# Performance work log

Measured on AMD Instinct MI355X. Metric: run time of the kernel, lower is better.

## Reference

```python
import jax, jax.numpy as jnp
import numpy as np

DIM = 768
NUM_HEADS = 16
D = DIM // NUM_HEADS  # 48


def setup_inputs() -> dict:
    key = jax.random.key(0)
    ks = jax.random.split(key, 7)
    x = jax.random.normal(ks[0], (4, 4096, DIM), dtype=jnp.float32)
    # Linear weights stored as [in, out] for x @ W + b
    s = 1.0 / np.sqrt(DIM)
    Wq = jax.random.uniform(ks[1], (DIM, D), jnp.float32, -s, s)
    Wk = jax.random.uniform(ks[2], (DIM, D), jnp.float32, -s, s)
    Wv = jax.random.uniform(ks[3], (DIM, D), jnp.float32, -s, s)
    bq = jax.random.uniform(ks[4], (D,), jnp.float32, -s, s)
    bk = jax.random.uniform(ks[5], (D,), jnp.float32, -s, s)
    bv = jax.random.uniform(ks[6], (D,), jnp.float32, -s, s)
    return {"x": x, "Wq": Wq, "bq": bq, "Wk": Wk, "bk": bk, "Wv": Wv, "bv": bv}


def reference(x, Wq, bq, Wk, bk, Wv, bv):
    # q, k, v: [B, S, D]
    q = x @ Wq + bq
    k = x @ Wk + bk
    v = x @ Wv + bv
    scale = 1.0 / jnp.sqrt(jnp.asarray(D, dtype=q.dtype))
    # scores: [B, S_q, S_k]
    scores = jnp.einsum("bqd,bkd->bqk", q, k) * scale
    # NOTE: softmax over dim=1 = the QUERY axis (faithful to original torch code)
    qk = jax.nn.softmax(scores, axis=1)
    # dropout is identity in eval mode (deterministic reference)
    attn = jnp.einsum("bqk,bkd->bqd", qk, v)
    return attn
```

## Files before the change

### kernel.cpp

```cpp
#include <hip/hip_runtime.h>
#include <hip/hip_bf16.h>

#define NB 4
#define SEQ 4096
#define CDIM 768
#define HD 48

typedef __attribute__((ext_vector_type(8))) __bf16 bf16x8;
typedef __attribute__((ext_vector_type(16))) float f32x16;

static constexpr float SCALE_LOG2E = 0.20823542135164923f;

__device__ __forceinline__ bf16x8 ldg8(const __hip_bfloat16* p) {
    uint4 u = *reinterpret_cast<const uint4*>(p);
    bf16x8 r;
    __builtin_memcpy(&r, &u, 16);
    return r;
}
__device__ __forceinline__ unsigned pk2(float lo, float hi) {
    const __hip_bfloat16 a = __float2bfloat16(lo);
    const __hip_bfloat16 b = __float2bfloat16(hi);
    unsigned short ua, ub;
    __builtin_memcpy(&ua, &a, 2);
    __builtin_memcpy(&ub, &b, 2);
    return (unsigned)ua | ((unsigned)ub << 16);
}
__device__ __forceinline__ bf16x8 mk8(unsigned w0, unsigned w1, unsigned w2, unsigned w3) {
    const uint4 u = make_uint4(w0, w1, w2, w3);
    bf16x8 r;
    __builtin_memcpy(&r, &u, 16);
    return r;
}
__device__ __forceinline__ void plswap(unsigned& a, unsigned& b) {
    asm volatile("v_permlane32_swap_b32 %0, %1" : "+v"(a), "+v"(b));
}
__device__ __forceinline__ size_t fragOff(int tile, int s, int h) {
    return (((size_t)tile * 3 + s) * 2 + h) * 256;
}

__global__ __launch_bounds__(256) void prep_kernel(
    const float* __restrict__ Wq, const float* __restrict__ Wk,
    const float* __restrict__ Wv,
    const float* __restrict__ bq, const float* __restrict__ bk,
    const float* __restrict__ bv,
    __hip_bfloat16* __restrict__ Wf, float* __restrict__ bias)
{
    const int g = blockIdx.x * 256 + threadIdx.x;
    if (g < 15360) {
        const int rem  = g % 3072;
        const int nt   = g / 3072;
        const int ks   = rem >> 6;
        const int l2   = rem & 63;
        const int hh   = l2 >> 5;
        const int lane = l2 & 31;
        const int n    = nt * 32 + lane;
        const float* src = (n < 48) ? Wq : (n < 96) ? Wk : (n < 144) ? Wv : nullptr;
        const int col = (n < 48) ? n : (n < 96) ? (n - 48) : (n - 96);
        #pragma unroll
        for (int j = 0; j < 8; ++j) {
            const int k = ks * 16 + hh * 8 + j;
            const float wv = src ? src[(size_t)k * HD + col] : 0.0f;
            Wf[(size_t)g * 8 + j] = __float2bfloat16(wv);
        }
    }
    if (blockIdx.x == 0 && threadIdx.x < 160) {
        const int t = threadIdx.x;
        bias[t] = (t < 48) ? bq[t] : (t < 96) ? bk[t - 48] : (t < 144) ? bv[t - 96] : 0.0f;
    }
}

__global__ __launch_bounds__(320) void proj_kernel(
    const float* __restrict__ x,
    const __hip_bfloat16* __restrict__ Wf, const float* __restrict__ bias,
    __hip_bfloat16* __restrict__ Qf, __hip_bfloat16* __restrict__ Kf,
    float* __restrict__ Vf)
{
    __shared__ __hip_bfloat16 xs[48 * 512];

    const int t   = threadIdx.x;
    const int w   = t >> 6;
    const int l   = t & 63;
    const int lo5 = l & 31, h = l >> 5;
    const int mt  = blockIdx.x;
    const int m0  = mt * 32;

    const float* xb = x + (size_t)m0 * CDIM;
    #pragma unroll
    for (int i = 0; i < 20; ++i) {
        const int c = i * 320 + t;
        if (c < 6144) {
            const int r   = c / 192;
            const int pos = c % 192;
            const int k   = pos * 4;
            const float4 v = *reinterpret_cast<const float4*>(xb + (size_t)r * CDIM + k);
            const int ks = k >> 4, hh = (k >> 3) & 1, j = k & 7;
            const uint2 d = make_uint2(pk2(v.x, v.y), pk2(v.z, v.w));
            *reinterpret_cast<uint2*>(&xs[ks * 512 + (hh * 32 + r) * 8 + j]) = d;
        }
    }
    __syncthreads();

    const __hip_bfloat16* bp = Wf + (size_t)w * 24576 + l * 8;
    f32x16 acc = {};
    #pragma unroll 8
    for (int ks = 0; ks < 48; ++ks) {
        bf16x8 a;
        __builtin_memcpy(&a, &xs[ks * 512 + l * 8], 16);
        const bf16x8 b = ldg8(bp + (size_t)ks * 512);
        __builtin_amdgcn_s_setprio(1);
        acc = __builtin_amdgcn_mfma_f32_32x32x16_bf16(a, b, acc, 0, 0, 0);
        __builtin_amdgcn_s_setprio(0);
    }

    const int n_g = w * 32 + lo5;
    const float bs = bias[n_g];
    if (n_g < 96) {
        const bool isQ = (n_g < 48);
        const int d  = isQ ? n_g : n_g - 48;
        const int s  = d >> 4;
        const int hf = (d >> 3) & 1;
        __hip_bfloat16* base = (isQ ? Qf : Kf) + fragOff(mt, s, hf) + (d & 7);
        #pragma unroll
        for (int r = 0; r < 16; ++r) {
            const int mrow = (r & 3) + 8 * (r >> 2) + 4 * h;
            float val = acc[r] + bs;
            if (isQ) val *= SCALE_LOG2E;
            base[mrow * 8] = __float2bfloat16(val);
        }
    } else if (n_g < 144) {
        const int d = n_g - 96;
        #pragma unroll
        for (int r = 0; r < 16; ++r) {
            const int m = m0 + (r & 3) + 8 * (r >> 2) + 4 * h;
            Vf[(size_t)m * HD + d] = acc[r] + bs;
        }
    }
}

__global__ __launch_bounds__(512) void stats_kernel(
    const __hip_bfloat16* __restrict__ Qf, const __hip_bfloat16* __restrict__ Kf,
    const float* __restrict__ Vf, __hip_bfloat16* __restrict__ Vt)
{
    __shared__ float part[8][32];
    __shared__ float linv[32];

    const int t   = threadIdx.x;
    const int w   = t >> 6;
    const int l   = t & 63;
    const int lo5 = l & 31, h = l >> 5;
    const int b       = blockIdx.y;
    const int ktile_l = blockIdx.x;
    const int ktile   = b * 128 + ktile_l;

    bf16x8 ka[3];
    #pragma unroll
    for (int s = 0; s < 3; ++s)
        ka[s] = ldg8(Kf + fragOff(ktile, s, h) + lo5 * 8);

    float lsum[16];
    #pragma unroll
    for (int r = 0; r < 16; ++r) lsum[r] = 0.0f;

    const int qt0 = b * 128 + w * 16;
    #pragma unroll 2
    for (int qq = 0; qq < 16; ++qq) {
        bf16x8 qb[3];
        #pragma unroll
        for (int s = 0; s < 3; ++s)
            qb[s] = ldg8(Qf + fragOff(qt0 + qq, s, h) + lo5 * 8);
        f32x16 acc = {};
        __builtin_amdgcn_s_setprio(1);
        #pragma unroll
        for (int s = 0; s < 3; ++s)
            acc = __builtin_amdgcn_mfma_f32_32x32x16_bf16(ka[s], qb[s], acc, 0, 0, 0);
        __builtin_amdgcn_s_setprio(0);
        #pragma unroll
        for (int r = 0; r < 16; ++r) lsum[r] += __builtin_amdgcn_exp2f(acc[r]);
    }

    #pragma unroll
    for (int r = 0; r < 16; ++r) {
        lsum[r] += __shfl_xor(lsum[r], 1);
        lsum[r] += __shfl_xor(lsum[r], 2);
        lsum[r] += __shfl_xor(lsum[r], 4);
        lsum[r] += __shfl_xor(lsum[r], 8);
        lsum[r] += __shfl_xor(lsum[r], 16);
    }
    if (lo5 == 0) {
        #pragma unroll
        for (int r = 0; r < 16; ++r)
            part[w][(r & 3) + 8 * (r >> 2) + 4 * h] = lsum[r];
    }
    __syncthreads();
    if (t < 32) {
        float s = 0.0f;
        #pragma unroll
        for (int p = 0; p < 8; ++p) s += part[p][t];
        linv[t] = 1.0f / s;
    }
    __syncthreads();

    const int kp = t & 15;
    const int dg = t >> 4;
    const float f0 = linv[2 * kp], f1 = linv[2 * kp + 1];
    __hip_bfloat16* vtb = Vt + (size_t)ktile * 2048;
    const float* vfb = Vf + ((size_t)b * SEQ + ktile_l * 32 + 2 * kp) * HD;
    {
        const int d = dg;
        const float v0 = vfb[d], v1 = vfb[HD + d];
        *reinterpret_cast<unsigned*>(&vtb[d * 32 + 2 * kp]) = pk2(v0 * f0, v1 * f1);
    }
    if (dg < 16) {
        const int d = dg + 32;
        const float v0 = vfb[d], v1 = vfb[HD + d];
        *reinterpret_cast<unsigned*>(&vtb[d * 32 + 2 * kp]) = pk2(v0 * f0, v1 * f1);
    }
}

__global__ __launch_bounds__(512) void pv_kernel(
    const __hip_bfloat16* __restrict__ Qf, const __hip_bfloat16* __restrict__ Kf,
    const __hip_bfloat16* __restrict__ Vt, float* __restrict__ out)
{
    __shared__ float red[8][32][64];

    const int t   = threadIdx.x;
    const int w   = t >> 6;
    const int l   = t & 63;
    const int lo5 = l & 31, h = l >> 5;
    const int b       = blockIdx.y;
    const int qtile_l = blockIdx.x;
    const int qtile   = b * 128 + qtile_l;
    const int q0      = qtile_l * 32;

    bf16x8 qb[3];
    #pragma unroll
    for (int s = 0; s < 3; ++s)
        qb[s] = ldg8(Qf + fragOff(qtile, s, h) + lo5 * 8);

    f32x16 o0 = {}, o1 = {};
    const int kt0 = b * 128 + w * 16;

    #pragma unroll 2
    for (int kk = 0; kk < 16; ++kk) {
        const int ktg = kt0 + kk;
        bf16x8 ka[3];
        #pragma unroll
        for (int s = 0; s < 3; ++s)
            ka[s] = ldg8(Kf + fragOff(ktg, s, h) + lo5 * 8);
        f32x16 acc = {};
        __builtin_amdgcn_s_setprio(1);
        #pragma unroll
        for (int s = 0; s < 3; ++s)
            acc = __builtin_amdgcn_mfma_f32_32x32x16_bf16(ka[s], qb[s], acc, 0, 0, 0);
        __builtin_amdgcn_s_setprio(0);

        float p[16];
        #pragma unroll
        for (int r = 0; r < 16; ++r) p[r] = __builtin_amdgcn_exp2f(acc[r]);

        unsigned w0 = pk2(p[0],  p[1]),  w1 = pk2(p[2],  p[3]);
        unsigned w2 = pk2(p[4],  p[5]),  w3 = pk2(p[6],  p[7]);
        unsigned w4 = pk2(p[8],  p[9]),  w5 = pk2(p[10], p[11]);
        unsigned w6 = pk2(p[12], p[13]), w7 = pk2(p[14], p[15]);
        plswap(w0, w2);
        plswap(w1, w3);
        plswap(w4, w6);
        plswap(w5, w7);

        const bf16x8 pa0 = mk8(w0, w1, w2, w3);
        const bf16x8 pa1 = mk8(w4, w5, w6, w7);

        const __hip_bfloat16* vt = Vt + (size_t)ktg * 2048 + lo5 * 32 + 8 * h;
        const bf16x8 va  = ldg8(vt);
        const bf16x8 vb2 = ldg8(vt + 16);
        const bf16x8 vc  = ldg8(vt + 1024);
        const bf16x8 vd  = ldg8(vt + 1024 + 16);
        __builtin_amdgcn_s_setprio(1);
        o0 = __builtin_amdgcn_mfma_f32_32x32x16_bf16(pa0, va,  o0, 0, 0, 0);
        o0 = __builtin_amdgcn_mfma_f32_32x32x16_bf16(pa1, vb2, o0, 0, 0, 0);
        o1 = __builtin_amdgcn_mfma_f32_32x32x16_bf16(pa0, vc,  o1, 0, 0, 0);
        o1 = __builtin_amdgcn_mfma_f32_32x32x16_bf16(pa1, vd,  o1, 0, 0, 0);
        __builtin_amdgcn_s_setprio(0);
    }

    #pragma unroll
    for (int r = 0; r < 16; ++r) {
        red[w][r][l]      = o0[r];
        red[w][16 + r][l] = o1[r];
    }
    __syncthreads();

    {
        const int rr = t >> 4;
        const int l0 = (t & 15) * 4;
        float4 s = make_float4(0.f, 0.f, 0.f, 0.f);
        #pragma unroll
        for (int p = 0; p < 8; ++p) {
            const float4 v = *reinterpret_cast<const float4*>(&red[p][rr][l0]);
            s.x += v.x; s.y += v.y; s.z += v.z; s.w += v.w;
        }
        const int r   = rr & 15;
        const int row = (r & 3) + 8 * (r >> 2) + 4 * (l0 >> 5);
        if (rr < 16) {
            *reinterpret_cast<float4*>(
                &out[((size_t)(b * SEQ) + q0 + row) * HD + (l0 & 31)]) = s;
        } else if ((l0 & 31) < 16) {
            *reinterpret_cast<float4*>(
                &out[((size_t)(b * SEQ) + q0 + row) * HD + 32 + (l0 & 31)]) = s;
        }
    }
}

extern "C" void kernel_launch(void* const* d_in, const int* in_sizes, int n_in,
                              void* d_out, int out_size, void* d_ws, size_t ws_size,
                              hipStream_t stream)
{
    const float* x  = (const float*)d_in[0];
    const float* Wq = (const float*)d_in[1];
    const float* bq = (const float*)d_in[2];
    const float* Wk = (const float*)d_in[3];
    const float* bk = (const float*)d_in[4];
    const float* Wv = (const float*)d_in[5];
    const float* bv = (const float*)d_in[6];
    float* out = (float*)d_out;

    const size_t FRAG = (size_t)512 * 6 * 256;
    __hip_bfloat16* Qf  = (__hip_bfloat16*)d_ws;
    __hip_bfloat16* Kf  = Qf + FRAG;
    float*          Vf  = (float*)(Kf + FRAG);
    __hip_bfloat16* Vt  = (__hip_bfloat16*)(Vf + (size_t)NB * SEQ * HD);
    __hip_bfloat16* Wf  = Vt + (size_t)NB * 128 * 2048;
    float*          bias = (float*)(Wf + (size_t)5 * 48 * 512);

    prep_kernel<<<dim3(60), 256, 0, stream>>>(Wq, Wk, Wv, bq, bk, bv, Wf, bias);
    proj_kernel<<<dim3(512), 320, 0, stream>>>(x, Wf, bias, Qf, Kf, Vf);
    stats_kernel<<<dim3(128, NB), 512, 0, stream>>>(Qf, Kf, Vf, Vt);
    pv_kernel<<<dim3(128, NB), 512, 0, stream>>>(Qf, Kf, Vt, out);
}
```

Before: 68.35 us.

## Process two tiles per block in stats/pv kernels with XCD-aware block remap

Each block of the stats and pv kernels now handles two 32-row tiles (two K tiles for stats, two Q tiles for pv), so each loaded Q/K/V fragment feeds twice as many MFMAs. The grid drops from 512 to 256 blocks. A remap assigns each batch to a pair of XCDs to improve L2 locality. The trade-offs are more registers per thread, fewer blocks to fill 256 CUs, and an extra reduction round through shared memory in pv.

```diff
diff --git a/kernel.cpp b/kernel.cpp
--- a/kernel.cpp
+++ b/kernel.cpp
@@ -36,6 +36,11 @@
 }
 __device__ __forceinline__ size_t fragOff(int tile, int s, int h) {
     return (((size_t)tile * 3 + s) * 2 + h) * 256;
+}
+__device__ __forceinline__ void xcd_remap64(int id, int& b, int& st) {
+    const int xcd = id & 7;
+    b  = xcd >> 1;
+    st = (xcd & 1) * 32 + (id >> 3);
 }
 
 __global__ __launch_bounds__(256) void prep_kernel(
@@ -137,29 +142,31 @@
     }
 }
 
-__global__ __launch_bounds__(512) void stats_kernel(
+__global__ __launch_bounds__(512, 2) void stats_kernel(
     const __hip_bfloat16* __restrict__ Qf, const __hip_bfloat16* __restrict__ Kf,
     const float* __restrict__ Vf, __hip_bfloat16* __restrict__ Vt)
 {
-    __shared__ float part[8][32];
-    __shared__ float linv[32];
+    __shared__ float part[8][64];
+    __shared__ float linv[64];
 
     const int t   = threadIdx.x;
     const int w   = t >> 6;
     const int l   = t & 63;
     const int lo5 = l & 31, h = l >> 5;
-    const int b       = blockIdx.y;
-    const int ktile_l = blockIdx.x;
-    const int ktile   = b * 128 + ktile_l;
-
-    bf16x8 ka[3];
-    #pragma unroll
-    for (int s = 0; s < 3; ++s)
-        ka[s] = ldg8(Kf + fragOff(ktile, s, h) + lo5 * 8);
-
-    float lsum[16];
-    #pragma unroll
-    for (int r = 0; r < 16; ++r) lsum[r] = 0.0f;
+    int b, kst;
+    xcd_remap64(blockIdx.x, b, kst);
+    const int ktile0 = b * 128 + kst * 2;
+
+    bf16x8 ka[6];
+    #pragma unroll
+    for (int s = 0; s < 3; ++s) {
+        ka[s]     = ldg8(Kf + fragOff(ktile0,     s, h) + lo5 * 8);
+        ka[3 + s] = ldg8(Kf + fragOff(ktile0 + 1, s, h) + lo5 * 8);
+    }
+
+    float lsum[32];
+    #pragma unroll
+    for (int r = 0; r < 32; ++r) lsum[r] = 0.0f;
 
     const int qt0 = b * 128 + w * 16;
     #pragma unroll 2
@@ -168,18 +175,24 @@
         #pragma unroll
         for (int s = 0; s < 3; ++s)
             qb[s] = ldg8(Qf + fragOff(qt0 + qq, s, h) + lo5 * 8);
-        f32x16 acc = {};
+        f32x16 a0 = {}, a1 = {};
         __builtin_amdgcn_s_setprio(1);
         #pragma unroll
         for (int s = 0; s < 3; ++s)
-            acc = __builtin_amdgcn_mfma_f32_32x32x16_bf16(ka[s], qb[s], acc, 0, 0, 0);
+            a0 = __builtin_amdgcn_mfma_f32_32x32x16_bf16(ka[s], qb[s], a0, 0, 0, 0);
+        #pragma unroll
+        for (int s = 0; s < 3; ++s)
+            a1 = __builtin_amdgcn_mfma_f32_32x32x16_bf16(ka[3 + s], qb[s], a1, 0, 0, 0);
         __builtin_amdgcn_s_setprio(0);
         #pragma unroll
-        for (int r = 0; r < 16; ++r) lsum[r] += __builtin_amdgcn_exp2f(acc[r]);
-    }
-
-    #pragma unroll
-    for (int r = 0; r < 16; ++r) {
+        for (int r = 0; r < 16; ++r) {
+            lsum[r]      += __builtin_amdgcn_exp2f(a0[r]);
+            lsum[16 + r] += __builtin_amdgcn_exp2f(a1[r]);
+        }
+    }
+
+    #pragma unroll
+    for (int r = 0; r < 32; ++r) {
         lsum[r] += __shfl_xor(lsum[r], 1);
         lsum[r] += __shfl_xor(lsum[r], 2);
         lsum[r] += __shfl_xor(lsum[r], 4);
@@ -188,11 +201,14 @@
     }
     if (lo5 == 0) {
         #pragma unroll
-        for (int r = 0; r < 16; ++r)
-            part[w][(r & 3) + 8 * (r >> 2) + 4 * h] = lsum[r];
+        for (int r = 0; r < 16; ++r) {
+            const int row = (r & 3) + 8 * (r >> 2) + 4 * h;
+            part[w][row]      = lsum[r];
+            part[w][32 + row] = lsum[16 + r];
+        }
     }
     __syncthreads();
-    if (t < 32) {
+    if (t < 64) {
         float s = 0.0f;
         #pragma unroll
         for (int p = 0; p < 8; ++p) s += part[p][t];
@@ -202,22 +218,26 @@
 
     const int kp = t & 15;
     const int dg = t >> 4;
-    const float f0 = linv[2 * kp], f1 = linv[2 * kp + 1];
-    __hip_bfloat16* vtb = Vt + (size_t)ktile * 2048;
-    const float* vfb = Vf + ((size_t)b * SEQ + ktile_l * 32 + 2 * kp) * HD;
-    {
-        const int d = dg;
-        const float v0 = vfb[d], v1 = vfb[HD + d];
-        *reinterpret_cast<unsigned*>(&vtb[d * 32 + 2 * kp]) = pk2(v0 * f0, v1 * f1);
-    }
-    if (dg < 16) {
-        const int d = dg + 32;
-        const float v0 = vfb[d], v1 = vfb[HD + d];
-        *reinterpret_cast<unsigned*>(&vtb[d * 32 + 2 * kp]) = pk2(v0 * f0, v1 * f1);
-    }
-}
-
-__global__ __launch_bounds__(512) void pv_kernel(
+    #pragma unroll
+    for (int tt = 0; tt < 2; ++tt) {
+        const int ktile = ktile0 + tt;
+        const float f0 = linv[tt * 32 + 2 * kp], f1 = linv[tt * 32 + 2 * kp + 1];
+        __hip_bfloat16* vtb = Vt + (size_t)ktile * 2048;
+        const float* vfb = Vf + ((size_t)b * SEQ + (kst * 2 + tt) * 32 + 2 * kp) * HD;
+        {
+            const int d = dg;
+            const float v0 = vfb[d], v1 = vfb[HD + d];
+            *reinterpret_cast<unsigned*>(&vtb[d * 32 + 2 * kp]) = pk2(v0 * f0, v1 * f1);
+        }
+        if (dg < 16) {
+            const int d = dg + 32;
+            const float v0 = vfb[d], v1 = vfb[HD + d];
+            *reinterpret_cast<unsigned*>(&vtb[d * 32 + 2 * kp]) = pk2(v0 * f0, v1 * f1);
+        }
+    }
+}
+
+__global__ __launch_bounds__(512, 2) void pv_kernel(
     const __hip_bfloat16* __restrict__ Qf, const __hip_bfloat16* __restrict__ Kf,
     const __hip_bfloat16* __restrict__ Vt, float* __restrict__ out)
 {
@@ -227,17 +247,19 @@
     const int w   = t >> 6;
     const int l   = t & 63;
     const int lo5 = l & 31, h = l >> 5;
-    const int b       = blockIdx.y;
-    const int qtile_l = blockIdx.x;
-    const int qtile   = b * 128 + qtile_l;
-    const int q0      = qtile_l * 32;
-
-    bf16x8 qb[3];
-    #pragma unroll
-    for (int s = 0; s < 3; ++s)
-        qb[s] = ldg8(Qf + fragOff(qtile, s, h) + lo5 * 8);
-
-    f32x16 o0 = {}, o1 = {};
+    int b, qst;
+    xcd_remap64(blockIdx.x, b, qst);
+    const int qtile0 = b * 128 + qst * 2;
+    const int q0     = qst * 64;
+
+    bf16x8 qb[6];
+    #pragma unroll
+    for (int s = 0; s < 3; ++s) {
+        qb[s]     = ldg8(Qf + fragOff(qtile0,     s, h) + lo5 * 8);
+        qb[3 + s] = ldg8(Qf + fragOff(qtile0 + 1, s, h) + lo5 * 8);
+    }
+
+    f32x16 o00 = {}, o01 = {}, o10 = {}, o11 = {};
     const int kt0 = b * 128 + w * 16;
 
     #pragma unroll 2
@@ -247,67 +269,84 @@
         #pragma unroll
         for (int s = 0; s < 3; ++s)
             ka[s] = ldg8(Kf + fragOff(ktg, s, h) + lo5 * 8);
-        f32x16 acc = {};
-        __builtin_amdgcn_s_setprio(1);
-        #pragma unroll
-        for (int s = 0; s < 3; ++s)
-            acc = __builtin_amdgcn_mfma_f32_32x32x16_bf16(ka[s], qb[s], acc, 0, 0, 0);
-        __builtin_amdgcn_s_setprio(0);
-
-        float p[16];
-        #pragma unroll
-        for (int r = 0; r < 16; ++r) p[r] = __builtin_amdgcn_exp2f(acc[r]);
-
-        unsigned w0 = pk2(p[0],  p[1]),  w1 = pk2(p[2],  p[3]);
-        unsigned w2 = pk2(p[4],  p[5]),  w3 = pk2(p[6],  p[7]);
-        unsigned w4 = pk2(p[8],  p[9]),  w5 = pk2(p[10], p[11]);
-        unsigned w6 = pk2(p[12], p[13]), w7 = pk2(p[14], p[15]);
-        plswap(w0, w2);
-        plswap(w1, w3);
-        plswap(w4, w6);
-        plswap(w5, w7);
-
-        const bf16x8 pa0 = mk8(w0, w1, w2, w3);
-        const bf16x8 pa1 = mk8(w4, w5, w6, w7);
-
         const __hip_bfloat16* vt = Vt + (size_t)ktg * 2048 + lo5 * 32 + 8 * h;
         const bf16x8 va  = ldg8(vt);
         const bf16x8 vb2 = ldg8(vt + 16);
         const bf16x8 vc  = ldg8(vt + 1024);
         const bf16x8 vd  = ldg8(vt + 1024 + 16);
-        __builtin_amdgcn_s_setprio(1);
-        o0 = __builtin_amdgcn_mfma_f32_32x32x16_bf16(pa0, va,  o0, 0, 0, 0);
-        o0 = __builtin_amdgcn_mfma_f32_32x32x16_bf16(pa1, vb2, o0, 0, 0, 0);
-        o1 = __builtin_amdgcn_mfma_f32_32x32x16_bf16(pa0, vc,  o1, 0, 0, 0);
-        o1 = __builtin_amdgcn_mfma_f32_32x32x16_bf16(pa1, vd,  o1, 0, 0, 0);
-        __builtin_amdgcn_s_setprio(0);
-    }
-
-    #pragma unroll
-    for (int r = 0; r < 16; ++r) {
-        red[w][r][l]      = o0[r];
-        red[w][16 + r][l] = o1[r];
-    }
-    __syncthreads();
-
-    {
-        const int rr = t >> 4;
-        const int l0 = (t & 15) * 4;
-        float4 s = make_float4(0.f, 0.f, 0.f, 0.f);
-        #pragma unroll
-        for (int p = 0; p < 8; ++p) {
-            const float4 v = *reinterpret_cast<const float4*>(&red[p][rr][l0]);
-            s.x += v.x; s.y += v.y; s.z += v.z; s.w += v.w;
-        }
-        const int r   = rr & 15;
-        const int row = (r & 3) + 8 * (r >> 2) + 4 * (l0 >> 5);
-        if (rr < 16) {
-            *reinterpret_cast<float4*>(
-                &out[((size_t)(b * SEQ) + q0 + row) * HD + (l0 & 31)]) = s;
-        } else if ((l0 & 31) < 16) {
-            *reinterpret_cast<float4*>(
-                &out[((size_t)(b * SEQ) + q0 + row) * HD + 32 + (l0 & 31)]) = s;
-        }
+
+        #pragma unroll
+        for (int qt = 0; qt < 2; ++qt) {
+            f32x16 acc = {};
+            __builtin_amdgcn_s_setprio(1);
+            #pragma unroll
+            for (int s = 0; s < 3; ++s)
+                acc = __builtin_amdgcn_mfma_f32_32x32x16_bf16(
+                    ka[s], qb[3 * qt + s], acc, 0, 0, 0);
+            __builtin_amdgcn_s_setprio(0);
+
+            float p[16];
+            #pragma unroll
+            for (int r = 0; r < 16; ++r) p[r] = __builtin_amdgcn_exp2f(acc[r]);
+
+            unsigned w0 = pk2(p[0],  p[1]),  w1 = pk2(p[2],  p[3]);
+            unsigned w2 = pk2(p[4],  p[5]),  w3 = pk2(p[6],  p[7]);
+            unsigned w4 = pk2(p[8],  p[9]),  w5 = pk2(p[10], p[11]);
+            unsigned w6 = pk2(p[12], p[13]), w7 = pk2(p[14], p[15]);
+            plswap(w0, w2);
+            plswap(w1, w3);
+            plswap(w4, w6);
+            plswap(w5, w7);
+            const bf16x8 pa0 = mk8(w0, w1, w2, w3);
+            const bf16x8 pa1 = mk8(w4, w5, w6, w7);
+
+            __builtin_amdgcn_s_setprio(1);
+            if (qt == 0) {
+                o00 = __builtin_amdgcn_mfma_f32_32x32x16_bf16(pa0, va,  o00, 0, 0, 0);
+                o00 = __builtin_amdgcn_mfma_f32_32x32x16_bf16(pa1, vb2, o00, 0, 0, 0);
+                o01 = __builtin_amdgcn_mfma_f32_32x32x16_bf16(pa0, vc,  o01, 0, 0, 0);
+                o01 = __builtin_amdgcn_mfma_f32_32x32x16_bf16(pa1, vd,  o01, 0, 0, 0);
+            } else {
+                o10 = __builtin_amdgcn_mfma_f32_32x32x16_bf16(pa0, va,  o10, 0, 0, 0);
+                o10 = __builtin_amdgcn_mfma_f32_32x32x16_bf16(pa1, vb2, o10, 0, 0, 0);
+                o11 = __builtin_amdgcn_mfma_f32_32x32x16_bf16(pa0, vc,  o11, 0, 0, 0);
+                o11 = __builtin_amdgcn_mfma_f32_32x32x16_bf16(pa1, vd,  o11, 0, 0, 0);
+            }
+            __builtin_amdgcn_s_setprio(0);
+        }
+    }
+
+    #pragma unroll
+    for (int round = 0; round < 2; ++round) {
+        const f32x16& a = round ? o10 : o00;
+        const f32x16& c = round ? o11 : o01;
+        #pragma unroll
+        for (int r = 0; r < 16; ++r) {
+            red[w][r][l]      = a[r];
+            red[w][16 + r][l] = c[r];
+        }
+        __syncthreads();
+        {
+            const int rr = t >> 4;
+            const int l0 = (t & 15) * 4;
+            float4 s = make_float4(0.f, 0.f, 0.f, 0.f);
+            #pragma unroll
+            for (int p = 0; p < 8; ++p) {
+                const float4 v = *reinterpret_cast<const float4*>(&red[p][rr][l0]);
+                s.x += v.x; s.y += v.y; s.z += v.z; s.w += v.w;
+            }
+            const int r    = rr & 15;
+            const int row  = (r & 3) + 8 * (r >> 2) + 4 * (l0 >> 5);
+            const int qrow = q0 + round * 32 + row;
+            if (rr < 16) {
+                *reinterpret_cast<float4*>(
+                    &out[((size_t)(b * SEQ) + qrow) * HD + (l0 & 31)]) = s;
+            } else if ((l0 & 31) < 16) {
+                *reinterpret_cast<float4*>(
+                    &out[((size_t)(b * SEQ) + qrow) * HD + 32 + (l0 & 31)]) = s;
+            }
+        }
+        __syncthreads();
     }
 }
 
@@ -334,6 +373,6 @@
 
     prep_kernel<<<dim3(60), 256, 0, stream>>>(Wq, Wk, Wv, bq, bk, bv, Wf, bias);
     proj_kernel<<<dim3(512), 320, 0, stream>>>(x, Wf, bias, Qf, Kf, Vf);
-    stats_kernel<<<dim3(128, NB), 512, 0, stream>>>(Qf, Kf, Vf, Vt);
-    pv_kernel<<<dim3(128, NB), 512, 0, stream>>>(Qf, Kf, Vt, out);
-}
+    stats_kernel<<<dim3(256), 512, 0, stream>>>(Qf, Kf, Vf, Vt);
+    pv_kernel<<<dim3(256), 512, 0, stream>>>(Qf, Kf, Vt, out);
+}
```

After: 65.51 us. -4.2%, faster.
